# Kernel optimization log

Measured on AMD Instinct MI355X. Metric: run time of the kernel, lower is better.

Reference implementation:

```python
import jax, jax.numpy as jnp
import numpy as np
from jax import lax

T, H, I, E, TOPK = 8192, 1024, 2048, 16, 2
IS = 2048  # shared-expert intermediate = intermediate_size * num_shared_experts


def setup_inputs() -> dict:
    key = jax.random.key(0)
    ks = jax.random.split(key, 6)
    s = lambda fan: 1.0 / np.sqrt(fan)
    return {
        "x": jax.random.normal(ks[0], (T, H), jnp.float32),
        "gate_w": jax.random.normal(ks[1], (H, E), jnp.float32) * s(H),
        "w1": jax.random.normal(ks[2], (E, H, 2 * I), jnp.float32) * s(H),
        "w2": jax.random.normal(ks[3], (E, I, H), jnp.float32) * s(I),
        "ws1": jax.random.normal(ks[4], (H, 2 * IS), jnp.float32) * s(H),
        "ws2": jax.random.normal(ks[5], (IS, H), jnp.float32) * s(IS),
    }


def _silu_and_mul(gu):
    g, u = jnp.split(gu, 2, axis=-1)
    return jax.nn.silu(g) * u


def reference(x, gate_w, w1, w2, ws1, ws2):
    # router: sigmoid -> top-k -> renormalize (token_choice_with_bias)
    logits = x @ gate_w                                   # [T, E]
    scores = jax.nn.sigmoid(logits.astype(jnp.float32))
    topk_w, topk_ids = lax.top_k(scores, TOPK)            # [T, K]
    topk_w = topk_w / jnp.sum(topk_w, axis=-1, keepdims=True)
    # scatter routing weights into dense combine matrix [T, E]
    combine = jnp.zeros((T, E), jnp.float32).at[
        jnp.arange(T)[:, None], topk_ids].set(topk_w).astype(x.dtype)

    # routed experts: scan over experts, accumulate weighted outputs
    def step(acc, inp):
        w1e, w2e, ce = inp                                # [H,2I], [I,H], [T]
        y = _silu_and_mul(x @ w1e) @ w2e                  # [T, H]
        return acc + ce[:, None] * y, None

    routed, _ = lax.scan(step, jnp.zeros_like(x), (w1, w2, combine.T))

    # shared expert (combination strategy = 'sum')
    shared = _silu_and_mul(x @ ws1) @ ws2                 # [T, H]
    return routed + shared
```

## Files before the change

kernel.cpp:

```cpp
#include <hip/hip_runtime.h>

#define T_TOK 8192
#define H_DIM 1024
#define E_NUM 16
#define I_DIM 2048
#define N1    4096
#define BK    64
#define MAX_TILES 208
#define MAX_ROWS (MAX_TILES * 128)

#define CTRL_COUNTS 0
#define CTRL_FILL   32
#define CTRL_OFFS   64
#define CTRL_TOTAL  96
#define CTRL_TE     128
#define CTRL_TR     (128 + MAX_TILES)
#define CTRL_INTS   (128 + 2 * MAX_TILES)

typedef __attribute__((ext_vector_type(8))) short short8;
typedef __attribute__((ext_vector_type(4))) float f32x4;

static const size_t OFF_WT1  = 0;
static const size_t OFF_WT2  = OFF_WT1  + (size_t)E_NUM * N1 * H_DIM * 2;
static const size_t OFF_WS1T = OFF_WT2  + (size_t)E_NUM * H_DIM * I_DIM * 2;
static const size_t OFF_WS2T = OFF_WS1T + (size_t)N1 * H_DIM * 2;
static const size_t OFF_XB   = OFF_WS2T + (size_t)I_DIM * H_DIM * 2;
static const size_t OFF_HID  = OFF_XB   + (size_t)T_TOK * H_DIM * 2;
static const size_t OFF_RIT  = OFF_HID  + (size_t)MAX_ROWS * I_DIM * 2;
static const size_t OFF_RIW  = OFF_RIT  + (size_t)MAX_ROWS * 4;
static const size_t OFF_CTRL = OFF_RIW  + (size_t)MAX_ROWS * 4;
static const size_t OFF_TKI  = OFF_CTRL + (size_t)CTRL_INTS * 4;
static const size_t OFF_TKW  = OFF_TKI  + (size_t)T_TOK * 2 * 4;

__device__ __forceinline__ unsigned short f2bf(float f) {
    unsigned int u = __float_as_uint(f);
    u = (u + 0x7FFFu + ((u >> 16) & 1u)) >> 16;
    return (unsigned short)u;
}

__global__ void transpose_cvt_kernel(const float* __restrict__ src,
                                     unsigned short* __restrict__ dst,
                                     int R, int C) {
    __shared__ float tile[64][65];
    const size_t base = (size_t)blockIdx.z * R * C;
    const int c0 = blockIdx.x * 64, r0 = blockIdx.y * 64;
    const int tid = threadIdx.x;
    #pragma unroll
    for (int i = 0; i < 16; i++) {
        int idx = tid + i * 256;
        int rl = idx >> 6, cl = idx & 63;
        tile[rl][cl] = src[base + (size_t)(r0 + rl) * C + (c0 + cl)];
    }
    __syncthreads();
    #pragma unroll
    for (int i = 0; i < 8; i++) {
        int p = tid + i * 256;
        int cr = p >> 5, h2 = (p & 31) * 2;
        unsigned int v = (unsigned int)f2bf(tile[h2][cr]) |
                         ((unsigned int)f2bf(tile[h2 + 1][cr]) << 16);
        *(unsigned int*)(dst + base + (size_t)(c0 + cr) * R + (r0 + h2)) = v;
    }
}

__global__ void cvt_x_kernel(const float* __restrict__ x, unsigned short* __restrict__ xb) {
    size_t i = (size_t)blockIdx.x * 256 + threadIdx.x;
    const float4* xp = (const float4*)x;
    float4 v0 = xp[i * 2], v1 = xp[i * 2 + 1];
    uint4 o;
    o.x = (unsigned)f2bf(v0.x) | ((unsigned)f2bf(v0.y) << 16);
    o.y = (unsigned)f2bf(v0.z) | ((unsigned)f2bf(v0.w) << 16);
    o.z = (unsigned)f2bf(v1.x) | ((unsigned)f2bf(v1.y) << 16);
    o.w = (unsigned)f2bf(v1.z) | ((unsigned)f2bf(v1.w) << 16);
    ((uint4*)xb)[i] = o;
}

__global__ void router_kernel(const float* __restrict__ x, const float* __restrict__ gw,
                              int* __restrict__ tki, float* __restrict__ tkw,
                              int* __restrict__ ctrl) {
    const int t = blockIdx.x;
    const int lane = threadIdx.x;
    float acc[16];
    #pragma unroll
    for (int e = 0; e < 16; e++) acc[e] = 0.f;
    const float* xr = x + (size_t)t * H_DIM;
    for (int h = lane; h < H_DIM; h += 64) {
        float xv = xr[h];
        const float4* g4 = (const float4*)(gw + h * 16);
        float4 a = g4[0], b = g4[1], c = g4[2], d = g4[3];
        acc[0] += xv * a.x; acc[1] += xv * a.y; acc[2]  += xv * a.z; acc[3]  += xv * a.w;
        acc[4] += xv * b.x; acc[5] += xv * b.y; acc[6]  += xv * b.z; acc[7]  += xv * b.w;
        acc[8] += xv * c.x; acc[9] += xv * c.y; acc[10] += xv * c.z; acc[11] += xv * c.w;
        acc[12]+= xv * d.x; acc[13]+= xv * d.y; acc[14] += xv * d.z; acc[15] += xv * d.w;
    }
    #pragma unroll
    for (int e = 0; e < 16; e++) {
        #pragma unroll
        for (int s = 32; s > 0; s >>= 1) acc[e] += __shfl_xor(acc[e], s);
    }
    if (lane == 0) {
        float sc[16];
        #pragma unroll
        for (int e = 0; e < 16; e++) sc[e] = 1.f / (1.f + __expf(-acc[e]));
        int i1 = 0;
        #pragma unroll
        for (int e = 1; e < 16; e++) if (sc[e] > sc[i1]) i1 = e;
        int i2 = (i1 == 0) ? 1 : 0;
        #pragma unroll
        for (int e = 0; e < 16; e++) if (e != i1 && sc[e] > sc[i2]) i2 = e;
        float s = sc[i1] + sc[i2];
        tki[2 * t] = i1; tki[2 * t + 1] = i2;
        tkw[2 * t] = sc[i1] / s; tkw[2 * t + 1] = sc[i2] / s;
        atomicAdd(&ctrl[CTRL_COUNTS + i1], 1);
        atomicAdd(&ctrl[CTRL_COUNTS + i2], 1);
    }
}

__global__ void prefix_kernel(int* __restrict__ ctrl) {
    if (threadIdx.x != 0) return;
    int off = 0, tc = 0;
    for (int e = 0; e <= 16; e++) {
        int c = (e == 16) ? T_TOK : ctrl[CTRL_COUNTS + e];
        ctrl[CTRL_OFFS + e] = off;
        int nt = (c + 127) >> 7;
        for (int i = 0; i < nt; i++) {
            ctrl[CTRL_TE + tc] = e;
            ctrl[CTRL_TR + tc] = off + i * 128;
            tc++;
        }
        off += nt << 7;
    }
    ctrl[CTRL_TOTAL] = tc;
}

__global__ void scatter_kernel(const int* __restrict__ tki, const float* __restrict__ tkw,
                               int* __restrict__ ctrl, int* __restrict__ rit,
                               float* __restrict__ riw) {
    int a = blockIdx.x * 256 + threadIdx.x;
    if (a < 2 * T_TOK) {
        int t = a >> 1;
        int e = tki[a];
        float w = tkw[a];
        int pos = atomicAdd(&ctrl[CTRL_FILL + e], 1);
        int row = ctrl[CTRL_OFFS + e] + pos;
        rit[row] = t; riw[row] = w;
    } else if (a < 3 * T_TOK) {
        int t = a - 2 * T_TOK;
        int row = ctrl[CTRL_OFFS + 16] + t;
        rit[row] = t; riw[row] = 1.0f;
    }
}

__global__ __launch_bounds__(256, 2)
void gemm1_kernel(const unsigned short* __restrict__ xb,
                  const unsigned short* __restrict__ wt1,
                  const unsigned short* __restrict__ ws1t,
                  unsigned short* __restrict__ hidden,
                  const int* __restrict__ rit,
                  const int* __restrict__ ctrl) {
    __shared__ float ldsf[16896];
    const int tile = blockIdx.x;
    if (tile >= ctrl[CTRL_TOTAL]) return;
    const int e    = ctrl[CTRL_TE + tile];
    const int row0 = ctrl[CTRL_TR + tile];
    const int n0   = blockIdx.y * 64;
    const unsigned short* bt = (e < 16) ? (wt1 + (size_t)e * N1 * H_DIM) : ws1t;

    unsigned short* sA = (unsigned short*)ldsf;
    unsigned short* sB = sA + 128 * BK;

    const int tid = threadIdx.x;
    const int lane = tid & 63;
    const int w = tid >> 6, wm = w >> 1, wn = w & 1;
    const int l15 = lane & 15;
    const int lk8 = (lane >> 4) * 8;

    int s_row[4]; int s_swz[4]; size_t a_base[4], b_base[4];
    #pragma unroll
    for (int i = 0; i < 4; i++) {
        int c = tid + 256 * i;
        int row = c >> 3;
        int k8 = (c & 7) * 8;
        s_row[i] = row;
        int byte = row * 128 + k8 * 2;
        s_swz[i] = byte ^ ((row & 7) << 4);
        int token = rit[row0 + row];
        a_base[i] = (size_t)token * H_DIM + k8;
        int gn = (row < 64) ? (n0 + row) : (2048 + n0 + row - 64);
        b_base[i] = (size_t)gn * H_DIM + k8;
    }

    f32x4 acc[4][4];
    #pragma unroll
    for (int a = 0; a < 4; a++)
        #pragma unroll
        for (int b = 0; b < 4; b++) acc[a][b] = (f32x4){0.f, 0.f, 0.f, 0.f};

    for (int k0 = 0; k0 < H_DIM; k0 += BK) {
        #pragma unroll
        for (int i = 0; i < 4; i++) {
            uint4 va = *(const uint4*)(xb + a_base[i] + k0);
            uint4 vb = *(const uint4*)(bt + b_base[i] + k0);
            *(uint4*)((char*)sA + s_swz[i]) = va;
            *(uint4*)((char*)sB + s_swz[i]) = vb;
        }
        __syncthreads();
        #pragma unroll
        for (int kk = 0; kk < 2; kk++) {
            short8 af[4], bfr[4];
            #pragma unroll
            for (int mi = 0; mi < 4; mi++) {
                int row = wm * 64 + mi * 16 + l15;
                int byte = row * 128 + (kk * 32 + lk8) * 2;
                af[mi] = *(const short8*)((const char*)sA + (byte ^ ((row & 7) << 4)));
            }
            #pragma unroll
            for (int ni = 0; ni < 4; ni++) {
                int row = wn * 64 + ni * 16 + l15;
                int byte = row * 128 + (kk * 32 + lk8) * 2;
                bfr[ni] = *(const short8*)((const char*)sB + (byte ^ ((row & 7) << 4)));
            }
            #pragma unroll
            for (int mi = 0; mi < 4; mi++)
                #pragma unroll
                for (int ni = 0; ni < 4; ni++)
                    acc[mi][ni] = __builtin_amdgcn_mfma_f32_16x16x32_bf16(
                        af[mi], bfr[ni], acc[mi][ni], 0, 0, 0);
        }
        __syncthreads();
    }

    float* ldsC = ldsf;
    const int crow = (lane >> 4) * 4;
    #pragma unroll
    for (int mi = 0; mi < 4; mi++)
        #pragma unroll
        for (int ni = 0; ni < 4; ni++) {
            int row = wm * 64 + mi * 16 + crow;
            int col = wn * 64 + ni * 16 + l15;
            #pragma unroll
            for (int r = 0; r < 4; r++)
                ldsC[(row + r) * 132 + col] = acc[mi][ni][r];
        }
    __syncthreads();
    #pragma unroll
    for (int i = 0; i < 8; i++) {
        int p = tid + i * 256;
        int row = p >> 4;
        int q = (p & 15) * 4;
        float4 g = *(const float4*)&ldsC[row * 132 + q];
        float4 u = *(const float4*)&ldsC[row * 132 + 64 + q];
        float a0 = g.x / (1.f + __expf(-g.x)) * u.x;
        float a1 = g.y / (1.f + __expf(-g.y)) * u.y;
        float a2 = g.z / (1.f + __expf(-g.z)) * u.z;
        float a3 = g.w / (1.f + __expf(-g.w)) * u.w;
        ushort4 hv;
        hv.x = f2bf(a0); hv.y = f2bf(a1); hv.z = f2bf(a2); hv.w = f2bf(a3);
        *(ushort4*)(hidden + (size_t)(row0 + row) * I_DIM + n0 + q) = hv;
    }
}

__global__ __launch_bounds__(256, 2)
void gemm2_kernel(const unsigned short* __restrict__ hidden,
                  const unsigned short* __restrict__ wt2,
                  const unsigned short* __restrict__ ws2t,
                  float* __restrict__ out,
                  const int* __restrict__ rit, const float* __restrict__ riw,
                  const int* __restrict__ ctrl) {
    __shared__ float ldsf[8192];
    const int tile = blockIdx.x;
    if (tile >= ctrl[CTRL_TOTAL]) return;
    const int e    = ctrl[CTRL_TE + tile];
    const int row0 = ctrl[CTRL_TR + tile];
    const int n0   = blockIdx.y * 128;
    const unsigned short* bt = (e < 16) ? (wt2 + (size_t)e * H_DIM * I_DIM) : ws2t;

    unsigned short* sA = (unsigned short*)ldsf;
    unsigned short* sB = sA + 128 * BK;

    const int tid = threadIdx.x;
    const int lane = tid & 63;
    const int w = tid >> 6, wm = w >> 1, wn = w & 1;
    const int l15 = lane & 15;
    const int lk8 = (lane >> 4) * 8;

    int s_swz[4]; size_t a_base[4], b_base[4];
    #pragma unroll
    for (int i = 0; i < 4; i++) {
        int c = tid + 256 * i;
        int row = c >> 3;
        int k8 = (c & 7) * 8;
        int byte = row * 128 + k8 * 2;
        s_swz[i] = byte ^ ((row & 7) << 4);
        a_base[i] = (size_t)(row0 + row) * I_DIM + k8;
        b_base[i] = (size_t)(n0 + row) * I_DIM + k8;
    }

    f32x4 acc[4][4];
    #pragma unroll
    for (int a = 0; a < 4; a++)
        #pragma unroll
        for (int b = 0; b < 4; b++) acc[a][b] = (f32x4){0.f, 0.f, 0.f, 0.f};

    for (int k0 = 0; k0 < I_DIM; k0 += BK) {
        #pragma unroll
        for (int i = 0; i < 4; i++) {
            uint4 va = *(const uint4*)(hidden + a_base[i] + k0);
            uint4 vb = *(const uint4*)(bt + b_base[i] + k0);
            *(uint4*)((char*)sA + s_swz[i]) = va;
            *(uint4*)((char*)sB + s_swz[i]) = vb;
        }
        __syncthreads();
        #pragma unroll
        for (int kk = 0; kk < 2; kk++) {
            short8 af[4], bfr[4];
            #pragma unroll
            for (int mi = 0; mi < 4; mi++) {
                int row = wm * 64 + mi * 16 + l15;
                int byte = row * 128 + (kk * 32 + lk8) * 2;
                af[mi] = *(const short8*)((const char*)sA + (byte ^ ((row & 7) << 4)));
            }
            #pragma unroll
            for (int ni = 0; ni < 4; ni++) {
                int row = wn * 64 + ni * 16 + l15;
                int byte = row * 128 + (kk * 32 + lk8) * 2;
                bfr[ni] = *(const short8*)((const char*)sB + (byte ^ ((row & 7) << 4)));
            }
            #pragma unroll
            for (int mi = 0; mi < 4; mi++)
                #pragma unroll
                for (int ni = 0; ni < 4; ni++)
                    acc[mi][ni] = __builtin_amdgcn_mfma_f32_16x16x32_bf16(
                        af[mi], bfr[ni], acc[mi][ni], 0, 0, 0);
        }
        __syncthreads();
    }

    const int crow = (lane >> 4) * 4;
    #pragma unroll
    for (int mi = 0; mi < 4; mi++) {
        int rowb = wm * 64 + mi * 16 + crow;
        #pragma unroll
        for (int r = 0; r < 4; r++) {
            int grow = row0 + rowb + r;
            int token = rit[grow];
            float wt = riw[grow];
            if (wt != 0.0f) {
                float* op = out + (size_t)token * H_DIM + n0;
                #pragma unroll
                for (int ni = 0; ni < 4; ni++) {
                    int col = wn * 64 + ni * 16 + l15;
                    atomicAdd(op + col, wt * acc[mi][ni][r]);
                }
            }
        }
    }
}

extern "C" void kernel_launch(void* const* d_in, const int* in_sizes, int n_in,
                              void* d_out, int out_size, void* d_ws, size_t ws_size,
                              hipStream_t stream) {
    const float* x      = (const float*)d_in[0];
    const float* gate_w = (const float*)d_in[1];
    const float* w1     = (const float*)d_in[2];
    const float* w2     = (const float*)d_in[3];
    const float* ws1    = (const float*)d_in[4];
    const float* ws2    = (const float*)d_in[5];
    float* out = (float*)d_out;
    char* ws = (char*)d_ws;

    unsigned short* wt1  = (unsigned short*)(ws + OFF_WT1);
    unsigned short* wt2  = (unsigned short*)(ws + OFF_WT2);
    unsigned short* ws1t = (unsigned short*)(ws + OFF_WS1T);
    unsigned short* ws2t = (unsigned short*)(ws + OFF_WS2T);
    unsigned short* xb   = (unsigned short*)(ws + OFF_XB);
    unsigned short* hid  = (unsigned short*)(ws + OFF_HID);
    int*   rit  = (int*)(ws + OFF_RIT);
    float* riw  = (float*)(ws + OFF_RIW);
    int*   ctrl = (int*)(ws + OFF_CTRL);
    int*   tki  = (int*)(ws + OFF_TKI);
    float* tkw  = (float*)(ws + OFF_TKW);

    hipMemsetAsync(d_out, 0, (size_t)T_TOK * H_DIM * sizeof(float), stream);
    hipMemsetAsync(ws + OFF_RIT, 0, OFF_TKI - OFF_RIT, stream);

    transpose_cvt_kernel<<<dim3(N1 / 64, H_DIM / 64, E_NUM), 256, 0, stream>>>(w1, wt1, H_DIM, N1);
    transpose_cvt_kernel<<<dim3(H_DIM / 64, I_DIM / 64, E_NUM), 256, 0, stream>>>(w2, wt2, I_DIM, H_DIM);
    transpose_cvt_kernel<<<dim3(N1 / 64, H_DIM / 64, 1), 256, 0, stream>>>(ws1, ws1t, H_DIM, N1);
    transpose_cvt_kernel<<<dim3(H_DIM / 64, I_DIM / 64, 1), 256, 0, stream>>>(ws2, ws2t, I_DIM, H_DIM);
    cvt_x_kernel<<<(T_TOK * H_DIM / 8) / 256, 256, 0, stream>>>(x, xb);

    router_kernel<<<T_TOK, 64, 0, stream>>>(x, gate_w, tki, tkw, ctrl);
    prefix_kernel<<<1, 64, 0, stream>>>(ctrl);
    scatter_kernel<<<(3 * T_TOK + 255) / 256, 256, 0, stream>>>(tki, tkw, ctrl, rit, riw);

    gemm1_kernel<<<dim3(MAX_TILES, N1 / 2 / 64), 256, 0, stream>>>(xb, wt1, ws1t, hid, rit, ctrl);
    gemm2_kernel<<<dim3(MAX_TILES, H_DIM / 128), 256, 0, stream>>>(hid, wt2, ws2t, out, rit, riw, ctrl);
}
```

Baseline: 1.355 ms.

## Use direct global-to-LDS loads, XCD-aware block swizzle, and fused register epilogue

The GEMM kernels now stage tiles with global_load_lds 16-byte direct loads into unswizzled LDS, which removes the register round trip. They also flatten the grid into a 1D launch with an XCD-aware remap, so blocks sharing a tile land on the same chiplet's L2. In gemm1 the B rows are interleaved so gate and up columns fall in the same wave's accumulators, letting SiLU*mul run from registers without the LDS staging epilogue. The transpose kernel also moves to float4 loads and 16-byte stores. Dropping the XOR swizzle may bring back LDS bank conflicts on fragment reads, and the epilogue now writes 2-byte scattered stores.

Result: faster. 1.252 ms (-7.6%).

```diff
diff --git a/kernel.cpp b/kernel.cpp
--- a/kernel.cpp
+++ b/kernel.cpp
@@ -8,6 +8,8 @@
 #define BK    64
 #define MAX_TILES 208
 #define MAX_ROWS (MAX_TILES * 128)
+#define YB1   32
+#define YB2   8
 
 #define CTRL_COUNTS 0
 #define CTRL_FILL   32
@@ -38,6 +40,12 @@
     return (unsigned short)u;
 }
 
+typedef __attribute__((address_space(1))) const void gv1_t;
+typedef __attribute__((address_space(3))) void lv3_t;
+__device__ __forceinline__ void gload16(const void* g, void* l) {
+    __builtin_amdgcn_global_load_lds((gv1_t*)g, (lv3_t*)l, 16, 0, 0);
+}
+
 __global__ void transpose_cvt_kernel(const float* __restrict__ src,
                                      unsigned short* __restrict__ dst,
                                      int R, int C) {
@@ -45,20 +53,27 @@
     const size_t base = (size_t)blockIdx.z * R * C;
     const int c0 = blockIdx.x * 64, r0 = blockIdx.y * 64;
     const int tid = threadIdx.x;
-    #pragma unroll
-    for (int i = 0; i < 16; i++) {
-        int idx = tid + i * 256;
-        int rl = idx >> 6, cl = idx & 63;
-        tile[rl][cl] = src[base + (size_t)(r0 + rl) * C + (c0 + cl)];
+    const int lr = tid >> 4;
+    const int lc = (tid & 15) * 4;
+    #pragma unroll
+    for (int i = 0; i < 4; i++) {
+        int r = lr + i * 16;
+        float4 v = *(const float4*)&src[base + (size_t)(r0 + r) * C + (c0 + lc)];
+        tile[r][lc] = v.x; tile[r][lc + 1] = v.y; tile[r][lc + 2] = v.z; tile[r][lc + 3] = v.w;
     }
     __syncthreads();
     #pragma unroll
-    for (int i = 0; i < 8; i++) {
+    for (int i = 0; i < 2; i++) {
         int p = tid + i * 256;
-        int cr = p >> 5, h2 = (p & 31) * 2;
-        unsigned int v = (unsigned int)f2bf(tile[h2][cr]) |
-                         ((unsigned int)f2bf(tile[h2 + 1][cr]) << 16);
-        *(unsigned int*)(dst + base + (size_t)(c0 + cr) * R + (r0 + h2)) = v;
+        int c = p >> 3;
+        int r8 = (p & 7) * 8;
+        unsigned int h[8];
+        #pragma unroll
+        for (int j = 0; j < 8; j++) h[j] = f2bf(tile[r8 + j][c]);
+        uint4 o;
+        o.x = h[0] | (h[1] << 16); o.y = h[2] | (h[3] << 16);
+        o.z = h[4] | (h[5] << 16); o.w = h[6] | (h[7] << 16);
+        *(uint4*)(dst + base + (size_t)(c0 + c) * R + (r0 + r8)) = o;
     }
 }
 
@@ -150,6 +165,12 @@
     }
 }
 
+__device__ __forceinline__ int xcd_swz(int id, int live) {
+    int xcd = id & 7, off = id >> 3;
+    int q = live >> 3, rr = live & 7;
+    return (xcd < rr ? xcd * (q + 1) : rr * (q + 1) + (xcd - rr) * q) + off;
+}
+
 __global__ __launch_bounds__(256, 2)
 void gemm1_kernel(const unsigned short* __restrict__ xb,
                   const unsigned short* __restrict__ wt1,
@@ -157,37 +178,38 @@
                   unsigned short* __restrict__ hidden,
                   const int* __restrict__ rit,
                   const int* __restrict__ ctrl) {
-    __shared__ float ldsf[16896];
-    const int tile = blockIdx.x;
-    if (tile >= ctrl[CTRL_TOTAL]) return;
+    __shared__ unsigned short sA[128 * BK];
+    __shared__ unsigned short sB[128 * BK];
+    const int total = ctrl[CTRL_TOTAL];
+    const int live = total * YB1;
+    int id = blockIdx.x;
+    if (id >= live) return;
+    id = xcd_swz(id, live);
+    const int tile = id >> 5;
+    const int n0 = (id & 31) * 64;
     const int e    = ctrl[CTRL_TE + tile];
     const int row0 = ctrl[CTRL_TR + tile];
-    const int n0   = blockIdx.y * 64;
     const unsigned short* bt = (e < 16) ? (wt1 + (size_t)e * N1 * H_DIM) : ws1t;
-
-    unsigned short* sA = (unsigned short*)ldsf;
-    unsigned short* sB = sA + 128 * BK;
 
     const int tid = threadIdx.x;
     const int lane = tid & 63;
     const int w = tid >> 6, wm = w >> 1, wn = w & 1;
     const int l15 = lane & 15;
     const int lk8 = (lane >> 4) * 8;
-
-    int s_row[4]; int s_swz[4]; size_t a_base[4], b_base[4];
+    const int k8 = (tid & 7) * 8;
+
+    const unsigned short* gA[4];
+    const unsigned short* gB[4];
     #pragma unroll
     for (int i = 0; i < 4; i++) {
-        int c = tid + 256 * i;
-        int row = c >> 3;
-        int k8 = (c & 7) * 8;
-        s_row[i] = row;
-        int byte = row * 128 + k8 * 2;
-        s_swz[i] = byte ^ ((row & 7) << 4);
-        int token = rit[row0 + row];
-        a_base[i] = (size_t)token * H_DIM + k8;
-        int gn = (row < 64) ? (n0 + row) : (2048 + n0 + row - 64);
-        b_base[i] = (size_t)gn * H_DIM + k8;
-    }
+        int r = i * 32 + (tid >> 3);
+        gA[i] = xb + (size_t)rit[row0 + r] * H_DIM + k8;
+        int half = (r >> 4) & 1, cg = r >> 5;
+        int gn = half * I_DIM + n0 + cg * 16 + (r & 15);
+        gB[i] = bt + (size_t)gn * H_DIM + k8;
+    }
+    char* lA = (char*)sA + (tid & 192) * 16;
+    char* lB = (char*)sB + (tid & 192) * 16;
 
     f32x4 acc[4][4];
     #pragma unroll
@@ -197,28 +219,21 @@
 
     for (int k0 = 0; k0 < H_DIM; k0 += BK) {
         #pragma unroll
-        for (int i = 0; i < 4; i++) {
-            uint4 va = *(const uint4*)(xb + a_base[i] + k0);
-            uint4 vb = *(const uint4*)(bt + b_base[i] + k0);
-            *(uint4*)((char*)sA + s_swz[i]) = va;
-            *(uint4*)((char*)sB + s_swz[i]) = vb;
-        }
+        for (int i = 0; i < 4; i++) gload16(gA[i] + k0, lA + i * 4096);
+        #pragma unroll
+        for (int i = 0; i < 4; i++) gload16(gB[i] + k0, lB + i * 4096);
         __syncthreads();
         #pragma unroll
         for (int kk = 0; kk < 2; kk++) {
             short8 af[4], bfr[4];
             #pragma unroll
-            for (int mi = 0; mi < 4; mi++) {
-                int row = wm * 64 + mi * 16 + l15;
-                int byte = row * 128 + (kk * 32 + lk8) * 2;
-                af[mi] = *(const short8*)((const char*)sA + (byte ^ ((row & 7) << 4)));
-            }
-            #pragma unroll
-            for (int ni = 0; ni < 4; ni++) {
-                int row = wn * 64 + ni * 16 + l15;
-                int byte = row * 128 + (kk * 32 + lk8) * 2;
-                bfr[ni] = *(const short8*)((const char*)sB + (byte ^ ((row & 7) << 4)));
-            }
+            for (int mi = 0; mi < 4; mi++)
+                af[mi] = *(const short8*)((const char*)sA +
+                          (wm * 64 + mi * 16 + l15) * 128 + kk * 64 + lk8 * 2);
+            #pragma unroll
+            for (int ni = 0; ni < 4; ni++)
+                bfr[ni] = *(const short8*)((const char*)sB +
+                          (wn * 64 + ni * 16 + l15) * 128 + kk * 64 + lk8 * 2);
             #pragma unroll
             for (int mi = 0; mi < 4; mi++)
                 #pragma unroll
@@ -229,33 +244,21 @@
         __syncthreads();
     }
 
-    float* ldsC = ldsf;
     const int crow = (lane >> 4) * 4;
     #pragma unroll
-    for (int mi = 0; mi < 4; mi++)
-        #pragma unroll
-        for (int ni = 0; ni < 4; ni++) {
-            int row = wm * 64 + mi * 16 + crow;
-            int col = wn * 64 + ni * 16 + l15;
-            #pragma unroll
-            for (int r = 0; r < 4; r++)
-                ldsC[(row + r) * 132 + col] = acc[mi][ni][r];
-        }
-    __syncthreads();
-    #pragma unroll
-    for (int i = 0; i < 8; i++) {
-        int p = tid + i * 256;
-        int row = p >> 4;
-        int q = (p & 15) * 4;
-        float4 g = *(const float4*)&ldsC[row * 132 + q];
-        float4 u = *(const float4*)&ldsC[row * 132 + 64 + q];
-        float a0 = g.x / (1.f + __expf(-g.x)) * u.x;
-        float a1 = g.y / (1.f + __expf(-g.y)) * u.y;
-        float a2 = g.z / (1.f + __expf(-g.z)) * u.z;
-        float a3 = g.w / (1.f + __expf(-g.w)) * u.w;
-        ushort4 hv;
-        hv.x = f2bf(a0); hv.y = f2bf(a1); hv.z = f2bf(a2); hv.w = f2bf(a3);
-        *(ushort4*)(hidden + (size_t)(row0 + row) * I_DIM + n0 + q) = hv;
+    for (int mi = 0; mi < 4; mi++) {
+        int rowb = row0 + wm * 64 + mi * 16 + crow;
+        #pragma unroll
+        for (int p = 0; p < 2; p++) {
+            int col = n0 + (wn * 2 + p) * 16 + l15;
+            f32x4 g = acc[mi][2 * p], u = acc[mi][2 * p + 1];
+            #pragma unroll
+            for (int r = 0; r < 4; r++) {
+                float gv = g[r];
+                float val = gv / (1.f + __expf(-gv)) * u[r];
+                hidden[(size_t)(rowb + r) * I_DIM + col] = f2bf(val);
+            }
+        }
     }
 }
 
@@ -266,34 +269,36 @@
                   float* __restrict__ out,
                   const int* __restrict__ rit, const float* __restrict__ riw,
                   const int* __restrict__ ctrl) {
-    __shared__ float ldsf[8192];
-    const int tile = blockIdx.x;
-    if (tile >= ctrl[CTRL_TOTAL]) return;
+    __shared__ unsigned short sA[128 * BK];
+    __shared__ unsigned short sB[128 * BK];
+    const int total = ctrl[CTRL_TOTAL];
+    const int live = total * YB2;
+    int id = blockIdx.x;
+    if (id >= live) return;
+    id = xcd_swz(id, live);
+    const int tile = id >> 3;
+    const int n0 = (id & 7) * 128;
     const int e    = ctrl[CTRL_TE + tile];
     const int row0 = ctrl[CTRL_TR + tile];
-    const int n0   = blockIdx.y * 128;
     const unsigned short* bt = (e < 16) ? (wt2 + (size_t)e * H_DIM * I_DIM) : ws2t;
-
-    unsigned short* sA = (unsigned short*)ldsf;
-    unsigned short* sB = sA + 128 * BK;
 
     const int tid = threadIdx.x;
     const int lane = tid & 63;
     const int w = tid >> 6, wm = w >> 1, wn = w & 1;
     const int l15 = lane & 15;
     const int lk8 = (lane >> 4) * 8;
-
-    int s_swz[4]; size_t a_base[4], b_base[4];
+    const int k8 = (tid & 7) * 8;
+
+    const unsigned short* gA[4];
+    const unsigned short* gB[4];
     #pragma unroll
     for (int i = 0; i < 4; i++) {
-        int c = tid + 256 * i;
-        int row = c >> 3;
-        int k8 = (c & 7) * 8;
-        int byte = row * 128 + k8 * 2;
-        s_swz[i] = byte ^ ((row & 7) << 4);
-        a_base[i] = (size_t)(row0 + row) * I_DIM + k8;
-        b_base[i] = (size_t)(n0 + row) * I_DIM + k8;
-    }
+        int r = i * 32 + (tid >> 3);
+        gA[i] = hidden + (size_t)(row0 + r) * I_DIM + k8;
+        gB[i] = bt + (size_t)(n0 + r) * I_DIM + k8;
+    }
+    char* lA = (char*)sA + (tid & 192) * 16;
+    char* lB = (char*)sB + (tid & 192) * 16;
 
     f32x4 acc[4][4];
     #pragma unroll
@@ -303,28 +308,21 @@
 
     for (int k0 = 0; k0 < I_DIM; k0 += BK) {
         #pragma unroll
-        for (int i = 0; i < 4; i++) {
-            uint4 va = *(const uint4*)(hidden + a_base[i] + k0);
-            uint4 vb = *(const uint4*)(bt + b_base[i] + k0);
-            *(uint4*)((char*)sA + s_swz[i]) = va;
-            *(uint4*)((char*)sB + s_swz[i]) = vb;
-        }
+        for (int i = 0; i < 4; i++) gload16(gA[i] + k0, lA + i * 4096);
+        #pragma unroll
+        for (int i = 0; i < 4; i++) gload16(gB[i] + k0, lB + i * 4096);
         __syncthreads();
         #pragma unroll
         for (int kk = 0; kk < 2; kk++) {
             short8 af[4], bfr[4];
             #pragma unroll
-            for (int mi = 0; mi < 4; mi++) {
-                int row = wm * 64 + mi * 16 + l15;
-                int byte = row * 128 + (kk * 32 + lk8) * 2;
-                af[mi] = *(const short8*)((const char*)sA + (byte ^ ((row & 7) << 4)));
-            }
-            #pragma unroll
-            for (int ni = 0; ni < 4; ni++) {
-                int row = wn * 64 + ni * 16 + l15;
-                int byte = row * 128 + (kk * 32 + lk8) * 2;
-                bfr[ni] = *(const short8*)((const char*)sB + (byte ^ ((row & 7) << 4)));
-            }
+            for (int mi = 0; mi < 4; mi++)
+                af[mi] = *(const short8*)((const char*)sA +
+                          (wm * 64 + mi * 16 + l15) * 128 + kk * 64 + lk8 * 2);
+            #pragma unroll
+            for (int ni = 0; ni < 4; ni++)
+                bfr[ni] = *(const short8*)((const char*)sB +
+                          (wn * 64 + ni * 16 + l15) * 128 + kk * 64 + lk8 * 2);
             #pragma unroll
             for (int mi = 0; mi < 4; mi++)
                 #pragma unroll
@@ -393,6 +391,6 @@
     prefix_kernel<<<1, 64, 0, stream>>>(ctrl);
     scatter_kernel<<<(3 * T_TOK + 255) / 256, 256, 0, stream>>>(tki, tkw, ctrl, rit, riw);
 
-    gemm1_kernel<<<dim3(MAX_TILES, N1 / 2 / 64), 256, 0, stream>>>(xb, wt1, ws1t, hid, rit, ctrl);
-    gemm2_kernel<<<dim3(MAX_TILES, H_DIM / 128), 256, 0, stream>>>(hid, wt2, ws2t, out, rit, riw, ctrl);
-}
+    gemm1_kernel<<<MAX_TILES * YB1, 256, 0, stream>>>(xb, wt1, ws1t, hid, rit, ctrl);
+    gemm2_kernel<<<MAX_TILES * YB2, 256, 0, stream>>>(hid, wt2, ws2t, out, rit, riw, ctrl);
+}
```
